# Performance work log

Measured on AMD Instinct MI355X. Metric: run time of the kernel, lower is better.

The kernel has to match this reference:

```python
import jax, jax.numpy as jnp
import numpy as np

T, H, W, N = 16, 1280, 1280, 64

def setup_inputs() -> dict:
    key = jax.random.key(0)
    k1, k2, k3 = jax.random.split(key, 3)
    result_data = jax.random.normal(k1, (T, H, W), dtype=jnp.float32)
    # boxes: (x1, y1, x2, y2) with x1 <= x2, y1 <= y2 (well-formed, as the torch code assumes)
    xs = jnp.sort(jax.random.randint(k2, (N, 2), 0, W, dtype=jnp.int32), axis=1)
    ys = jnp.sort(jax.random.randint(k3, (N, 2), 0, H, dtype=jnp.int32), axis=1)
    boxes_data = jnp.stack([xs[:, 0], ys[:, 0], xs[:, 1], ys[:, 1]], axis=1)  # [N,4]
    return {"result_data": result_data, "boxes_data": boxes_data}

def reference(result_data, boxes_data):
    # result_data: [T,H,W] float; boxes_data: [N,4] int (x1,y1,x2,y2), exclusive upper bounds.
    # Fuse all per-box region sums via a 2D integral image (summed-area table):
    # S[t, y, x] = sum(result_data[t, :y, :x]); box sum = S[y2,x2]-S[y1,x2]-S[y2,x1]+S[y1,x1].
    cs = jnp.cumsum(jnp.cumsum(result_data, axis=1), axis=2)          # [T,H,W]
    S = jnp.pad(cs, ((0, 0), (1, 0), (1, 0)))                          # [T,H+1,W+1]
    x1, y1, x2, y2 = boxes_data[:, 0], boxes_data[:, 1], boxes_data[:, 2], boxes_data[:, 3]
    box_sums = S[:, y2, x2] - S[:, y1, x2] - S[:, y2, x1] + S[:, y1, x1]  # [T,N]
    return box_sums.sum()
```

## Files before the change

### kernel.cpp

```cpp
#include <hip/hip_runtime.h>

#define TT 16
#define HH 1280
#define WW 1280
#define NBOX 64
#define W4 (WW / 4)
#define SLICE4 (HH * W4)

__global__ void build_masks_kernel(const int* __restrict__ boxes,
                                   unsigned long long* __restrict__ rowmask,
                                   unsigned long long* __restrict__ colmask) {
    __shared__ int bx1[NBOX], by1[NBOX], bx2[NBOX], by2[NBOX];
    int tid = threadIdx.x;
    if (tid < NBOX) {
        int4 b = ((const int4*)boxes)[tid];
        bx1[tid] = b.x; by1[tid] = b.y; bx2[tid] = b.z; by2[tid] = b.w;
    }
    __syncthreads();
    int g = blockIdx.x * 256 + tid;
    if (g < HH) {
        int y = g;
        unsigned long long m = 0ull;
#pragma unroll
        for (int b = 0; b < NBOX; ++b)
            if (by1[b] <= y && y < by2[b]) m |= (1ull << b);
        rowmask[y] = m;
    } else if (g < HH + WW) {
        int x = g - HH;
        unsigned long long m = 0ull;
#pragma unroll
        for (int b = 0; b < NBOX; ++b)
            if (bx1[b] <= x && x < bx2[b]) m |= (1ull << b);
        colmask[x] = m;
    }
}

__global__ void __launch_bounds__(256)
weighted_sum_kernel(const float4* __restrict__ data,
                    const unsigned long long* __restrict__ rowmask,
                    const longlong2* __restrict__ colmask2,
                    float* __restrict__ out) {
    int idx = blockIdx.x * 256 + threadIdx.x;
    int y  = idx / W4;
    int x4 = idx - y * W4;

    unsigned long long rm = rowmask[y];
    longlong2 c01 = colmask2[x4 * 2 + 0];
    longlong2 c23 = colmask2[x4 * 2 + 1];

    const float4* p = data + idx;
    float4 v[TT];
#pragma unroll
    for (int t = 0; t < TT; ++t)
        v[t] = p[t * SLICE4];

    __builtin_amdgcn_sched_barrier(0);

    float w0 = (float)__popcll(rm & (unsigned long long)c01.x);
    float w1 = (float)__popcll(rm & (unsigned long long)c01.y);
    float w2 = (float)__popcll(rm & (unsigned long long)c23.x);
    float w3 = (float)__popcll(rm & (unsigned long long)c23.y);

    float a0 = 0.f, a1 = 0.f, a2 = 0.f, a3 = 0.f;
#pragma unroll
    for (int t = 0; t < TT; t += 4) {
        a0 += v[t + 0].x * w0 + v[t + 0].y * w1 + v[t + 0].z * w2 + v[t + 0].w * w3;
        a1 += v[t + 1].x * w0 + v[t + 1].y * w1 + v[t + 1].z * w2 + v[t + 1].w * w3;
        a2 += v[t + 2].x * w0 + v[t + 2].y * w1 + v[t + 2].z * w2 + v[t + 2].w * w3;
        a3 += v[t + 3].x * w0 + v[t + 3].y * w1 + v[t + 3].z * w2 + v[t + 3].w * w3;
    }
    float acc = (a0 + a1) + (a2 + a3);

#pragma unroll
    for (int off = 32; off > 0; off >>= 1)
        acc += __shfl_down(acc, off, 64);

    __shared__ float wsum[4];
    int lane = threadIdx.x & 63;
    int wid  = threadIdx.x >> 6;
    if (lane == 0) wsum[wid] = acc;
    __syncthreads();
    if (threadIdx.x == 0) {
        float s = (wsum[0] + wsum[1]) + (wsum[2] + wsum[3]);
        atomicAdd(out, s);
    }
}

extern "C" void kernel_launch(void* const* d_in, const int* in_sizes, int n_in,
                              void* d_out, int out_size, void* d_ws, size_t ws_size,
                              hipStream_t stream) {
    const float* data = (const float*)d_in[0];
    const int* boxes  = (const int*)d_in[1];
    float* out = (float*)d_out;

    unsigned long long* rowmask = (unsigned long long*)d_ws;
    unsigned long long* colmask = rowmask + HH;

    hipMemsetAsync(out, 0, sizeof(float), stream);
    build_masks_kernel<<<10, 256, 0, stream>>>(boxes, rowmask, colmask);
    weighted_sum_kernel<<<SLICE4 / 256, 256, 0, stream>>>(
        (const float4*)data, rowmask, (const longlong2*)colmask, out);
}
```

Before: 157.6 us.

## Split time dimension across two thread groups, nontemporal loads, fold memset into mask kernel

Doubles the grid so each thread handles half of the T slices, giving each thread 8 loads instead of 16 in flight. Loads use nontemporal hints to avoid polluting cache with streamed data. The output zeroing moves from a separate memset into the mask-building kernel, removing one launch. More threads mean more mask loads and twice as many atomics.

```diff
diff --git a/kernel.cpp b/kernel.cpp
--- a/kernel.cpp
+++ b/kernel.cpp
@@ -6,16 +6,22 @@
 #define NBOX 64
 #define W4 (WW / 4)
 #define SLICE4 (HH * W4)
+#define TSPLIT 2
+#define TPT (TT / TSPLIT)
+
+typedef float f32x4 __attribute__((ext_vector_type(4)));
 
 __global__ void build_masks_kernel(const int* __restrict__ boxes,
                                    unsigned long long* __restrict__ rowmask,
-                                   unsigned long long* __restrict__ colmask) {
+                                   unsigned long long* __restrict__ colmask,
+                                   float* __restrict__ out) {
     __shared__ int bx1[NBOX], by1[NBOX], bx2[NBOX], by2[NBOX];
     int tid = threadIdx.x;
     if (tid < NBOX) {
         int4 b = ((const int4*)boxes)[tid];
         bx1[tid] = b.x; by1[tid] = b.y; bx2[tid] = b.z; by2[tid] = b.w;
     }
+    if (blockIdx.x == 0 && tid == 0) *out = 0.f;
     __syncthreads();
     int g = blockIdx.x * 256 + tid;
     if (g < HH) {
@@ -36,23 +42,25 @@
 }
 
 __global__ void __launch_bounds__(256)
-weighted_sum_kernel(const float4* __restrict__ data,
+weighted_sum_kernel(const f32x4* __restrict__ data,
                     const unsigned long long* __restrict__ rowmask,
                     const longlong2* __restrict__ colmask2,
                     float* __restrict__ out) {
     int idx = blockIdx.x * 256 + threadIdx.x;
-    int y  = idx / W4;
-    int x4 = idx - y * W4;
+    int tz  = (idx >= SLICE4) ? 1 : 0;
+    int pos = idx - tz * SLICE4;
+    int y  = pos / W4;
+    int x4 = pos - y * W4;
 
     unsigned long long rm = rowmask[y];
     longlong2 c01 = colmask2[x4 * 2 + 0];
     longlong2 c23 = colmask2[x4 * 2 + 1];
 
-    const float4* p = data + idx;
-    float4 v[TT];
+    const f32x4* p = data + tz * (TPT * SLICE4) + pos;
+    f32x4 v[TPT];
 #pragma unroll
-    for (int t = 0; t < TT; ++t)
-        v[t] = p[t * SLICE4];
+    for (int t = 0; t < TPT; ++t)
+        v[t] = __builtin_nontemporal_load(p + t * SLICE4);
 
     __builtin_amdgcn_sched_barrier(0);
 
@@ -63,7 +71,7 @@
 
     float a0 = 0.f, a1 = 0.f, a2 = 0.f, a3 = 0.f;
 #pragma unroll
-    for (int t = 0; t < TT; t += 4) {
+    for (int t = 0; t < TPT; t += 4) {
         a0 += v[t + 0].x * w0 + v[t + 0].y * w1 + v[t + 0].z * w2 + v[t + 0].w * w3;
         a1 += v[t + 1].x * w0 + v[t + 1].y * w1 + v[t + 1].z * w2 + v[t + 1].w * w3;
         a2 += v[t + 2].x * w0 + v[t + 2].y * w1 + v[t + 2].z * w2 + v[t + 2].w * w3;
@@ -96,8 +104,7 @@
     unsigned long long* rowmask = (unsigned long long*)d_ws;
     unsigned long long* colmask = rowmask + HH;
 
-    hipMemsetAsync(out, 0, sizeof(float), stream);
-    build_masks_kernel<<<10, 256, 0, stream>>>(boxes, rowmask, colmask);
-    weighted_sum_kernel<<<SLICE4 / 256, 256, 0, stream>>>(
-        (const float4*)data, rowmask, (const longlong2*)colmask, out);
+    build_masks_kernel<<<10, 256, 0, stream>>>(boxes, rowmask, colmask, out);
+    weighted_sum_kernel<<<(TSPLIT * SLICE4) / 256, 256, 0, stream>>>(
+        (const f32x4*)data, rowmask, (const longlong2*)colmask, out);
 }
```

Measured after the change: 177.6 us. 12.7% more time.
